# Performance work log

Hardware: AMD Instinct MI355X
Metric: run time of the kernel (lower is better)

## Reference

```python
import jax, jax.numpy as jnp
import numpy as np

H = 16
E = 2048
LAT = E // 4
D = E // H          # 128
R = D // 2          # 64 (rotary dim)
B, S = 2, 2048

def _lin(x, W, b):
    return x @ W.T + b

def _rope_cos_sin(seq_len):
    inv_freq = 1.0 / (10000.0 ** (jnp.arange(0, R, 2, dtype=jnp.float32) / R))  # (R/2,)
    t = jnp.arange(seq_len, dtype=jnp.float32)
    freqs = jnp.outer(t, inv_freq)                 # (S, R/2)
    emb = jnp.concatenate([freqs, freqs], axis=-1) # (S, R)
    return jnp.cos(emb), jnp.sin(emb)

def _rotate_half(x):
    x1, x2 = x[..., : R // 2], x[..., R // 2 :]
    return jnp.concatenate([-x2, x1], axis=-1)

def _apply_rope(x, cos, sin):
    # x: (B, S, H, R); cos/sin: (S, R)
    c = cos[None, :, None, :]
    s = sin[None, :, None, :]
    return x * c + _rotate_half(x) * s

def setup_inputs() -> dict:
    key = jax.random.key(0)
    ks = jax.random.split(key, 20)
    def w(k, o, i):
        return jax.random.normal(k, (o, i), dtype=jnp.float32) * 0.02
    def bvec(k, o):
        return jax.random.normal(k, (o,), dtype=jnp.float32) * 0.02
    return {
        "x": jax.random.normal(ks[0], (B, S, E), dtype=jnp.float32),
        "Wkv_d": w(ks[1], LAT, E), "bkv_d": bvec(ks[2], LAT),
        "Wq_d": w(ks[3], LAT, E), "bq_d": bvec(ks[4], LAT),
        "Wk_u": w(ks[5], E // 2, LAT), "bk_u": bvec(ks[6], E // 2),
        "Wq_u": w(ks[7], E // 2, LAT), "bq_u": bvec(ks[8], E // 2),
        "Wv_u": w(ks[9], E, LAT), "bv_u": bvec(ks[10], E),
        "Wrk": w(ks[11], E // 2, E), "brk": bvec(ks[12], E // 2),
        "Wrq": w(ks[13], E // 2, LAT), "brq": bvec(ks[14], E // 2),
        "Wo": w(ks[15], E, E), "bo": bvec(ks[16], E),
    }

def reference(x, Wkv_d, bkv_d, Wq_d, bq_d, Wk_u, bk_u, Wq_u, bq_u,
              Wv_u, bv_u, Wrk, brk, Wrq, brq, Wo, bo):
    Bn, Sn, _ = x.shape
    kv_d = _lin(x, Wkv_d, bkv_d)                      # (B,S,LAT)
    q_d = _lin(x, Wq_d, bq_d)                         # (B,S,LAT)
    k1 = _lin(kv_d, Wk_u, bk_u).reshape(Bn, Sn, H, R)
    q1 = _lin(q_d, Wq_u, bq_u).reshape(Bn, Sn, H, R)
    v = _lin(kv_d, Wv_u, bv_u).reshape(Bn, Sn, H, D)
    kr = _lin(x, Wrk, brk).reshape(Bn, Sn, H, R)
    qr = _lin(q_d, Wrq, brq).reshape(Bn, Sn, H, R)
    cos, sin = _rope_cos_sin(Sn)
    qr = _apply_rope(qr, cos, sin)
    kr = _apply_rope(kr, cos, sin)
    k = jnp.concatenate([k1, kr], axis=-1)            # (B,S,H,D)
    q = jnp.concatenate([q1, qr], axis=-1)
    scale = 1.0 / np.sqrt(D)
    attn = jnp.einsum("bqhd,bkhd->bhqk", q, k) * scale
    attn = jax.nn.softmax(attn, axis=-1)
    out = jnp.einsum("bhqk,bkhd->bqhd", attn, v).reshape(Bn, Sn, E)
    return _lin(out, Wo, bo)
```

## Files before the change

kernel.cpp:

```cpp
#include <hip/hip_runtime.h>
#include <cmath>

typedef unsigned short ushort_t;
typedef unsigned int u32;
typedef __attribute__((ext_vector_type(8))) __bf16 bf16x8;
typedef __attribute__((ext_vector_type(4))) float f32x4;

#define Hh 16
#define Ss 2048
#define SCALE 0.08838834764831845f

__device__ __forceinline__ ushort_t f2bf(float f) {
  union { float f; unsigned u; } c; c.f = f;
  unsigned u = c.u;
  return (ushort_t)((u + 0x7FFFu + ((u >> 16) & 1u)) >> 16);
}
__device__ __forceinline__ float bf2f(ushort_t h) {
  union { unsigned u; float f; } c; c.u = ((unsigned)h) << 16;
  return c.f;
}
__device__ __forceinline__ u32 cvt_pk_bf16(float lo, float hi) {
  u32 r;
  asm volatile("v_cvt_pk_bf16_f32 %0, %1, %2" : "=v"(r) : "v"(lo), "v"(hi));
  return r;
}

__device__ __forceinline__ void gload_lds16(const ushort_t* g, ushort_t* l) {
  __builtin_amdgcn_global_load_lds(
      (const __attribute__((address_space(1))) u32*)g,
      (__attribute__((address_space(3))) u32*)l, 16, 0, 0);
}

struct SrcPtrs { const float* p[16]; };

__global__ __launch_bounds__(256) void convert_all_kernel(SrcPtrs sp,
    ushort_t* __restrict__ x_bf, ushort_t* __restrict__ wbuf,
    float* __restrict__ biasbuf, float2* __restrict__ ropetb) {
  const int cum[16] = {8192, 9216, 10240, 12288, 12800, 13824, 14336, 14848,
                       18944, 18945, 18946, 18947, 18948, 18950, 18951, 18952};
  const int dsto[9] = {0, 0, 1048576, 2097152, 4194304, 4718592, 5767168, 6291456, 6815744};
  const int boff[7] = {0, 512, 1024, 2048, 3072, 5120, 6144};
  const int bsz[7]  = {512, 512, 1024, 1024, 2048, 1024, 1024};
  const int bid = blockIdx.x;
  int s = 0;
  #pragma unroll
  for (int i = 0; i < 16; ++i) s += (bid >= cum[i]);
  const int lb = bid - (s == 0 ? 0 : cum[s - 1]);
  if (s < 9) {
    const float* src = sp.p[s] + (size_t)lb * 1024;
    ushort_t* dst = (s == 0 ? x_bf : wbuf + dsto[s]) + (size_t)lb * 1024;
    const int i = threadIdx.x * 4;
    float4 v = *(const float4*)&src[i];
    ushort4 o;
    o.x = f2bf(v.x); o.y = f2bf(v.y); o.z = f2bf(v.z); o.w = f2bf(v.w);
    *(ushort4*)&dst[i] = o;
  } else if (s < 16) {
    const int k = s - 9;
    const int e = lb * 1024 + threadIdx.x * 4;
    if (e < bsz[k])
      *(float4*)&biasbuf[boff[k] + e] = *(const float4*)&sp.p[s][e];
  } else {
    const int i = lb * 256 + threadIdx.x;
    const int sq = i >> 5, ii = i & 31;
    const float invf = expf(-logf(10000.f) * (float)ii / 32.f);
    const float fr = (float)sq * invf;
    ropetb[i] = make_float2(cosf(fr), sinf(fr));
  }
}

template<int MODE, typename OUTT>
__global__ __launch_bounds__(256) void gemm_bf16(
    const ushort_t* __restrict__ A, const ushort_t* __restrict__ W,
    const float* __restrict__ bias, OUTT* __restrict__ C0,
    ushort_t* __restrict__ C1, ushort_t* __restrict__ C2,
    const float2* __restrict__ tb, int K)
{
  __shared__ ushort_t As[128][64];
  __shared__ ushort_t Bs[128][64];
  const int tid = threadIdx.x;
  const int lane = tid & 63;
  const int w = tid >> 6;
  const int wr = w >> 1, wc = w & 1;
  const int l15 = lane & 15, lhi = lane >> 4;
  const int m0 = blockIdx.y * 128, n0 = blockIdx.x * 128;

  if constexpr (MODE == 5) { if (blockIdx.x >= 24) A += 2097152; }

  const int srow_base = w * 8 + (lane >> 3);
  const int scol = (lane & 7) * 8;

  f32x4 acc[4][4];
  #pragma unroll
  for (int i = 0; i < 4; ++i)
    #pragma unroll
    for (int j = 0; j < 4; ++j)
      acc[i][j] = (f32x4){0.f, 0.f, 0.f, 0.f};

  for (int k0 = 0; k0 < K; k0 += 64) {
    __syncthreads();
    #pragma unroll
    for (int q = 0; q < 4; ++q) {
      const int row = q * 32 + srow_base;
      gload_lds16(&A[(size_t)(m0 + row) * K + k0 + scol], &As[q * 32 + w * 8][0]);
      gload_lds16(&W[(size_t)(n0 + row) * K + k0 + scol], &Bs[q * 32 + w * 8][0]);
    }
    __syncthreads();
    #pragma unroll
    for (int dk = 0; dk < 2; ++dk) {
      bf16x8 af[4], bfr[4];
      #pragma unroll
      for (int i = 0; i < 4; ++i)
        af[i] = *(const bf16x8*)&As[wr * 64 + i * 16 + l15][dk * 32 + lhi * 8];
      #pragma unroll
      for (int j = 0; j < 4; ++j)
        bfr[j] = *(const bf16x8*)&Bs[wc * 64 + j * 16 + l15][dk * 32 + lhi * 8];
      #pragma unroll
      for (int i = 0; i < 4; ++i)
        #pragma unroll
        for (int j = 0; j < 4; ++j)
          acc[i][j] = __builtin_amdgcn_mfma_f32_16x16x32_bf16(af[i], bfr[j], acc[i][j], 0, 0, 0);
    }
  }

  const bool rope_region =
      (MODE == 2 && blockIdx.x >= 8) || (MODE == 5 && blockIdx.x >= 32);

  if (rope_region) {
    #pragma unroll
    for (int i = 0; i < 4; ++i) {
      #pragma unroll
      for (int p = 0; p < 2; ++p) {
        const int nA = n0 + wc * 64 + p * 16 + l15;
        const int nB = nA + 32;
        const float bzA = bias[nA];
        const float bzB = bias[nB];
        int colA, colB;
        ushort_t* Cb;
        if constexpr (MODE == 2) {
          const int npA = nA - 1024;
          colA = (npA >> 6) * 128 + (npA & 63);
          colB = colA + 32;
          Cb = C1;
        } else {
          const int npA = nA - 4096;
          colA = (npA >> 6) * 128 + 64 + (npA & 63);
          colB = colA + 32;
          Cb = C2;
        }
        const int ii = p * 16 + l15;
        #pragma unroll
        for (int r = 0; r < 4; ++r) {
          const int m = m0 + wr * 64 + i * 16 + lhi * 4 + r;
          const int s = m & (Ss - 1);
          const float2 cs = tb[(s << 5) + ii];
          const float x1 = acc[i][p][r] + bzA;
          const float x2 = acc[i][p + 2][r] + bzB;
          Cb[(size_t)m * 2048 + colA] = f2bf(x1 * cs.x - x2 * cs.y);
          Cb[(size_t)m * 2048 + colB] = f2bf(x2 * cs.x + x1 * cs.y);
        }
      }
    }
    return;
  }

  #pragma unroll
  for (int i = 0; i < 4; ++i) {
    #pragma unroll
    for (int j = 0; j < 4; ++j) {
      const int n = n0 + wc * 64 + j * 16 + l15;
      const float bz = bias[n];
      #pragma unroll
      for (int r = 0; r < 4; ++r) {
        const int m = m0 + wr * 64 + i * 16 + lhi * 4 + r;
        const float v = acc[i][j][r] + bz;
        if constexpr (MODE == 0) {
          C0[(size_t)m * 2048 + n] = v;
        } else if constexpr (MODE == 2) {
          C0[(size_t)(n >> 9) * 2097152 + (size_t)m * 512 + (n & 511)] = (OUTT)f2bf(v);
        } else {
          if (n < 1024) {
            C0[(size_t)m * 2048 + (n >> 6) * 128 + (n & 63)] = (OUTT)f2bf(v);
          } else if (n < 3072) {
            const int np = n - 1024;
            C1[(size_t)(m >> 11) * 4194304 + (size_t)np * 2048 + (m & 2047)] = f2bf(v);
          } else {
            const int np = n - 3072;
            C2[(size_t)m * 2048 + (np >> 6) * 128 + (np & 63)] = f2bf(v);
          }
        }
      }
    }
  }
}

__global__ __launch_bounds__(256) void flash_mfma_kernel(
    const ushort_t* __restrict__ Qb, const ushort_t* __restrict__ Kb,
    const ushort_t* __restrict__ Vt, ushort_t* __restrict__ Oattn)
{
  __shared__ ushort_t Ks[64][128];
  __shared__ ushort_t Vs[128][64];
  __shared__ ushort_t Ps[4][32][64];

  const int tid = threadIdx.x, lane = tid & 63, w = tid >> 6;
  const int l15 = lane & 15, lhi = lane >> 4;
  const int l7 = l15 & 7;
  const int id = blockIdx.x;
  const int xcd = id & 7, chunk = id >> 3;
  const int qx = chunk & 15, bh = ((chunk >> 4) << 3) | xcd;
  const int b = bh >> 4, h = bh & 15;
  const int q0 = qx * 128 + w * 32;

  bf16x8 qf[2][4];
  #pragma unroll
  for (int mi = 0; mi < 2; ++mi) {
    const size_t qrow = (size_t)b * Ss + q0 + mi * 16 + l15;
    const ushort_t* qp = Qb + (qrow * Hh + h) * 128;
    #pragma unroll
    for (int dk = 0; dk < 4; ++dk)
      qf[mi][dk] = *(const bf16x8*)(qp + dk * 32 + lhi * 8);
  }

  f32x4 o[2][8];
  #pragma unroll
  for (int mi = 0; mi < 2; ++mi)
    #pragma unroll
    for (int dn = 0; dn < 8; ++dn) o[mi][dn] = (f32x4){0.f, 0.f, 0.f, 0.f};
  float lsum[2] = {0.f, 0.f};

  const size_t kbase_g = (size_t)b * Ss * 2048 + (size_t)h * 128;
  const size_t vbase_g = (size_t)bh * 128 * Ss;

  bf16x8 kv[4], vv[4];
  #pragma unroll
  for (int p = 0; p < 4; ++p) {
    const int idx = p * 256 + tid;
    kv[p] = *(const bf16x8*)&Kb[kbase_g + (size_t)(idx >> 4) * 2048 + (idx & 15) * 8];
    vv[p] = *(const bf16x8*)&Vt[vbase_g + (size_t)(idx >> 3) * Ss + (idx & 7) * 8];
  }

  for (int t = 0; t < Ss / 64; ++t) {
    __syncthreads();
    #pragma unroll
    for (int p = 0; p < 4; ++p) {
      const int idx = p * 256 + tid;
      const int kr = idx >> 4, kc = idx & 15;
      const int vr = idx >> 3, vc = idx & 7;
      *(bf16x8*)&Ks[kr][(kc ^ (kr & 7)) * 8] = kv[p];
      *(bf16x8*)&Vs[vr][(vc ^ (vr & 7)) * 8] = vv[p];
    }
    __syncthreads();

    if (t + 1 < Ss / 64) {
      const int s1 = (t + 1) * 64;
      #pragma unroll
      for (int p = 0; p < 4; ++p) {
        const int idx = p * 256 + tid;
        kv[p] = *(const bf16x8*)&Kb[kbase_g + (size_t)(s1 + (idx >> 4)) * 2048 + (idx & 15) * 8];
        vv[p] = *(const bf16x8*)&Vt[vbase_g + (size_t)(idx >> 3) * Ss + s1 + (idx & 7) * 8];
      }
    }

    f32x4 s[2][4];
    #pragma unroll
    for (int mi = 0; mi < 2; ++mi)
      #pragma unroll
      for (int jc = 0; jc < 4; ++jc) s[mi][jc] = (f32x4){0.f, 0.f, 0.f, 0.f};
    #pragma unroll
    for (int jc = 0; jc < 4; ++jc)
      #pragma unroll
      for (int dk = 0; dk < 4; ++dk) {
        bf16x8 ak = *(const bf16x8*)&Ks[jc * 16 + l15][((dk * 4 + lhi) ^ l7) * 8];
        s[0][jc] = __builtin_amdgcn_mfma_f32_16x16x32_bf16(ak, qf[0][dk], s[0][jc], 0, 0, 0);
        s[1][jc] = __builtin_amdgcn_mfma_f32_16x16x32_bf16(ak, qf[1][dk], s[1][jc], 0, 0, 0);
      }

    #pragma unroll
    for (int mi = 0; mi < 2; ++mi)
      #pragma unroll
      for (int jc = 0; jc < 4; ++jc) {
        const float p0 = __expf(s[mi][jc][0] * SCALE);
        const float p1 = __expf(s[mi][jc][1] * SCALE);
        const float p2 = __expf(s[mi][jc][2] * SCALE);
        const float p3 = __expf(s[mi][jc][3] * SCALE);
        lsum[mi] += (p0 + p1) + (p2 + p3);
        const u32 d0 = cvt_pk_bf16(p0, p1);
        const u32 d1 = cvt_pk_bf16(p2, p3);
        const int ch = (jc * 2 + (lhi >> 1)) ^ l7;
        *(uint2*)&Ps[w][mi * 16 + l15][ch * 8 + (lhi & 1) * 4] = make_uint2(d0, d1);
      }

    #pragma unroll
    for (int kc = 0; kc < 2; ++kc) {
      bf16x8 ap0 = *(const bf16x8*)&Ps[w][l15][((kc * 4 + lhi) ^ l7) * 8];
      bf16x8 ap1 = *(const bf16x8*)&Ps[w][16 + l15][((kc * 4 + lhi) ^ l7) * 8];
      #pragma unroll
      for (int dn = 0; dn < 8; ++dn) {
        bf16x8 bv = *(const bf16x8*)&Vs[dn * 16 + l15][((kc * 4 + lhi) ^ l7) * 8];
        o[0][dn] = __builtin_amdgcn_mfma_f32_16x16x32_bf16(ap0, bv, o[0][dn], 0, 0, 0);
        o[1][dn] = __builtin_amdgcn_mfma_f32_16x16x32_bf16(ap1, bv, o[1][dn], 0, 0, 0);
      }
    }
  }

  #pragma unroll
  for (int mi = 0; mi < 2; ++mi) {
    float v = lsum[mi];
    v += __shfl_xor(v, 16);
    v += __shfl_xor(v, 32);
    lsum[mi] = v;
  }

  #pragma unroll
  for (int mi = 0; mi < 2; ++mi) {
    float inv[4];
    #pragma unroll
    for (int r = 0; r < 4; ++r)
      inv[r] = 1.f / __shfl(lsum[mi], lhi * 4 + r);
    #pragma unroll
    for (int dn = 0; dn < 8; ++dn)
      #pragma unroll
      for (int r = 0; r < 4; ++r) {
        const int row = q0 + mi * 16 + lhi * 4 + r;
        const size_t addr = ((size_t)b * Ss + row) * 2048 + h * 128 + dn * 16 + l15;
        Oattn[addr] = f2bf(o[mi][dn][r] * inv[r]);
      }
  }
}

extern "C" void kernel_launch(void* const* d_in, const int* in_sizes, int n_in,
                              void* d_out, int out_size, void* d_ws, size_t ws_size,
                              hipStream_t stream)
{
  const float* x     = (const float*)d_in[0];
  const float* Wkv_d = (const float*)d_in[1];
  const float* bkv_d = (const float*)d_in[2];
  const float* Wq_d  = (const float*)d_in[3];
  const float* bq_d  = (const float*)d_in[4];
  const float* Wk_u  = (const float*)d_in[5];
  const float* bk_u  = (const float*)d_in[6];
  const float* Wq_u  = (const float*)d_in[7];
  const float* bq_u  = (const float*)d_in[8];
  const float* Wv_u  = (const float*)d_in[9];
  const float* bv_u  = (const float*)d_in[10];
  const float* Wrk   = (const float*)d_in[11];
  const float* brk   = (const float*)d_in[12];
  const float* Wrq   = (const float*)d_in[13];
  const float* brq   = (const float*)d_in[14];
  const float* Wo    = (const float*)d_in[15];
  const float* bo    = (const float*)d_in[16];

  ushort_t* ws = (ushort_t*)d_ws;
  ushort_t* x_bf  = ws;
  ushort_t* kv_d  = ws + 8388608;
  ushort_t* q_d   = ws + 10485760;
  ushort_t* qb    = ws + 12582912;
  ushort_t* kb    = ws + 20971520;
  ushort_t* vt    = ws + 29360128;
  ushort_t* attn  = ws + 37748736;
  ushort_t* wbuf  = ws + 46137344;
  float* biasbuf  = (float*)(ws + 57147392);
  float2* ropetb  = (float2*)(ws + 57161728);

  SrcPtrs sp;
  sp.p[0] = x;     sp.p[1] = Wkv_d; sp.p[2] = Wq_d;  sp.p[3] = Wrk;
  sp.p[4] = Wk_u;  sp.p[5] = Wv_u;  sp.p[6] = Wq_u;  sp.p[7] = Wrq;
  sp.p[8] = Wo;
  sp.p[9] = bkv_d; sp.p[10] = bq_d; sp.p[11] = brk;  sp.p[12] = bk_u;
  sp.p[13] = bv_u; sp.p[14] = bq_u; sp.p[15] = brq;
  convert_all_kernel<<<dim3(19208), dim3(256), 0, stream>>>(sp, x_bf, wbuf, biasbuf, ropetb);

  const dim3 blk(256);

  gemm_bf16<2, ushort_t><<<dim3(16, 32), blk, 0, stream>>>(
      x_bf, wbuf, biasbuf, kv_d, kb + 64, nullptr, ropetb, 2048);
  gemm_bf16<5, ushort_t><<<dim3(40, 32), blk, 0, stream>>>(
      kv_d, wbuf + 4194304, biasbuf + 2048, kb, vt, qb, ropetb, 512);

  flash_mfma_kernel<<<dim3(512), blk, 0, stream>>>(qb, kb, vt, attn);

  gemm_bf16<0, float><<<dim3(16, 32), blk, 0, stream>>>(
      attn, wbuf + 6815744, bo, (float*)d_out, nullptr, nullptr, nullptr, 2048);
}
```

Baseline: 265.9 us.

## Split attention over KV halves with a merge kernel for more blocks

Adds a split-KV path for flash attention: each (b,h,q-tile) is handled by two blocks, each covering half of the keys, which doubles the grid from 512 to 1024 blocks to fill more CUs. Each block writes unnormalized bf16 partial outputs and row sums, and a new merge kernel adds the halves and divides by the total sum. It works without max subtraction, as the original did, so the partials share a scale. In exchange it adds an extra kernel launch, extra global traffic for the partial outputs, and an extra bf16 rounding of the unnormalized partials. The path is chosen only when the workspace is large enough.

```diff
diff --git a/kernel.cpp b/kernel.cpp
--- a/kernel.cpp
+++ b/kernel.cpp
@@ -193,9 +193,11 @@
   }
 }
 
+template<int SPLIT>
 __global__ __launch_bounds__(256) void flash_mfma_kernel(
     const ushort_t* __restrict__ Qb, const ushort_t* __restrict__ Kb,
-    const ushort_t* __restrict__ Vt, ushort_t* __restrict__ Oattn)
+    const ushort_t* __restrict__ Vt, ushort_t* __restrict__ Out,
+    float* __restrict__ lpart)
 {
   __shared__ ushort_t Ks[64][128];
   __shared__ ushort_t Vs[128][64];
@@ -205,10 +207,17 @@
   const int l15 = lane & 15, lhi = lane >> 4;
   const int l7 = l15 & 7;
   const int id = blockIdx.x;
-  const int xcd = id & 7, chunk = id >> 3;
-  const int qx = chunk & 15, bh = ((chunk >> 4) << 3) | xcd;
+  const int xcd = id & 7, c = id >> 3;
+  int half, qx, bh;
+  if constexpr (SPLIT) {
+    half = c & 1; qx = (c >> 1) & 15; bh = ((c >> 5) << 3) | xcd;
+  } else {
+    half = 0; qx = c & 15; bh = ((c >> 4) << 3) | xcd;
+  }
   const int b = bh >> 4, h = bh & 15;
   const int q0 = qx * 128 + w * 32;
+  const int sbase = SPLIT ? half * 1024 : 0;
+  const int NT = SPLIT ? 16 : 32;
 
   bf16x8 qf[2][4];
   #pragma unroll
@@ -234,11 +243,11 @@
   #pragma unroll
   for (int p = 0; p < 4; ++p) {
     const int idx = p * 256 + tid;
-    kv[p] = *(const bf16x8*)&Kb[kbase_g + (size_t)(idx >> 4) * 2048 + (idx & 15) * 8];
-    vv[p] = *(const bf16x8*)&Vt[vbase_g + (size_t)(idx >> 3) * Ss + (idx & 7) * 8];
-  }
-
-  for (int t = 0; t < Ss / 64; ++t) {
+    kv[p] = *(const bf16x8*)&Kb[kbase_g + (size_t)(sbase + (idx >> 4)) * 2048 + (idx & 15) * 8];
+    vv[p] = *(const bf16x8*)&Vt[vbase_g + (size_t)(idx >> 3) * Ss + sbase + (idx & 7) * 8];
+  }
+
+  for (int t = 0; t < NT; ++t) {
     __syncthreads();
     #pragma unroll
     for (int p = 0; p < 4; ++p) {
@@ -250,8 +259,8 @@
     }
     __syncthreads();
 
-    if (t + 1 < Ss / 64) {
-      const int s1 = (t + 1) * 64;
+    if (t + 1 < NT) {
+      const int s1 = sbase + (t + 1) * 64;
       #pragma unroll
       for (int p = 0; p < 4; ++p) {
         const int idx = p * 256 + tid;
@@ -310,21 +319,63 @@
     lsum[mi] = v;
   }
 
-  #pragma unroll
-  for (int mi = 0; mi < 2; ++mi) {
-    float inv[4];
-    #pragma unroll
-    for (int r = 0; r < 4; ++r)
-      inv[r] = 1.f / __shfl(lsum[mi], lhi * 4 + r);
-    #pragma unroll
-    for (int dn = 0; dn < 8; ++dn)
-      #pragma unroll
-      for (int r = 0; r < 4; ++r) {
-        const int row = q0 + mi * 16 + lhi * 4 + r;
-        const size_t addr = ((size_t)b * Ss + row) * 2048 + h * 128 + dn * 16 + l15;
-        Oattn[addr] = f2bf(o[mi][dn][r] * inv[r]);
-      }
-  }
+  if constexpr (SPLIT) {
+    ushort_t* op = Out + (size_t)half * 8388608;
+    #pragma unroll
+    for (int mi = 0; mi < 2; ++mi) {
+      #pragma unroll
+      for (int dn = 0; dn < 8; ++dn)
+        #pragma unroll
+        for (int r = 0; r < 4; ++r) {
+          const int row = q0 + mi * 16 + lhi * 4 + r;
+          const size_t addr = ((size_t)b * Ss + row) * 2048 + h * 128 + dn * 16 + l15;
+          op[addr] = f2bf(o[mi][dn][r]);
+        }
+      if (lhi == 0)
+        lpart[half * 65536 + bh * 2048 + q0 + mi * 16 + l15] = lsum[mi];
+    }
+  } else {
+    #pragma unroll
+    for (int mi = 0; mi < 2; ++mi) {
+      float inv[4];
+      #pragma unroll
+      for (int r = 0; r < 4; ++r)
+        inv[r] = 1.f / __shfl(lsum[mi], lhi * 4 + r);
+      #pragma unroll
+      for (int dn = 0; dn < 8; ++dn)
+        #pragma unroll
+        for (int r = 0; r < 4; ++r) {
+          const int row = q0 + mi * 16 + lhi * 4 + r;
+          const size_t addr = ((size_t)b * Ss + row) * 2048 + h * 128 + dn * 16 + l15;
+          Out[addr] = f2bf(o[mi][dn][r] * inv[r]);
+        }
+    }
+  }
+}
+
+__global__ __launch_bounds__(256) void merge_kernel(
+    const ushort_t* __restrict__ opart, const float* __restrict__ lpart,
+    ushort_t* __restrict__ attn)
+{
+  const int e = (blockIdx.x * 256 + threadIdx.x) * 8;
+  const int h = (e >> 7) & 15, srow = (e >> 11) & 2047, b = e >> 22;
+  const int lidx = (((b << 4) | h) << 11) + srow;
+  const float inv = 1.f / (lpart[lidx] + lpart[65536 + lidx]);
+  ushort4 a0 = *(const ushort4*)&opart[e];
+  ushort4 a1 = *(const ushort4*)&opart[e + 4];
+  ushort4 b0 = *(const ushort4*)&opart[8388608 + e];
+  ushort4 b1 = *(const ushort4*)&opart[8388608 + e + 4];
+  ushort4 r0, r1;
+  r0.x = f2bf((bf2f(a0.x) + bf2f(b0.x)) * inv);
+  r0.y = f2bf((bf2f(a0.y) + bf2f(b0.y)) * inv);
+  r0.z = f2bf((bf2f(a0.z) + bf2f(b0.z)) * inv);
+  r0.w = f2bf((bf2f(a0.w) + bf2f(b0.w)) * inv);
+  r1.x = f2bf((bf2f(a1.x) + bf2f(b1.x)) * inv);
+  r1.y = f2bf((bf2f(a1.y) + bf2f(b1.y)) * inv);
+  r1.z = f2bf((bf2f(a1.z) + bf2f(b1.z)) * inv);
+  r1.w = f2bf((bf2f(a1.w) + bf2f(b1.w)) * inv);
+  *(ushort4*)&attn[e] = r0;
+  *(ushort4*)&attn[e + 4] = r1;
 }
 
 extern "C" void kernel_launch(void* const* d_in, const int* in_sizes, int n_in,
@@ -360,6 +411,9 @@
   ushort_t* wbuf  = ws + 46137344;
   float* biasbuf  = (float*)(ws + 57147392);
   float2* ropetb  = (float2*)(ws + 57161728);
+  ushort_t* opart = ws + 57423872;
+  float* lpart    = (float*)(ws + 74201088);
+  const size_t WS_NEED_SPLIT = 74463232ULL * 2ULL;
 
   SrcPtrs sp;
   sp.p[0] = x;     sp.p[1] = Wkv_d; sp.p[2] = Wq_d;  sp.p[3] = Wrk;
@@ -376,7 +430,12 @@
   gemm_bf16<5, ushort_t><<<dim3(40, 32), blk, 0, stream>>>(
       kv_d, wbuf + 4194304, biasbuf + 2048, kb, vt, qb, ropetb, 512);
 
-  flash_mfma_kernel<<<dim3(512), blk, 0, stream>>>(qb, kb, vt, attn);
+  if (ws_size >= WS_NEED_SPLIT) {
+    flash_mfma_kernel<1><<<dim3(1024), blk, 0, stream>>>(qb, kb, vt, opart, lpart);
+    merge_kernel<<<dim3(4096), blk, 0, stream>>>(opart, lpart, attn);
+  } else {
+    flash_mfma_kernel<0><<<dim3(512), blk, 0, stream>>>(qb, kb, vt, attn, nullptr);
+  }
 
   gemm_bf16<0, float><<<dim3(16, 32), blk, 0, stream>>>(
       attn, wbuf + 6815744, bo, (float*)d_out, nullptr, nullptr, nullptr, 2048);
```

Measured after the change: 276.9 us. 4.1% more time.
